# Kernel tuning notes

Measured on AMD Instinct MI355X. Metric: run time of the kernel, lower is better.

## Reference

```python
import jax, jax.numpy as jnp
import numpy as np

B, L, N, C = 8, 33600, 128, 80
ALPHA, BETA, TOPK, EPS = 1.0, 6.0, 13, 1e-9


def setup_inputs() -> dict:
    key = jax.random.key(0)
    ks = jax.random.split(key, 7)
    pred_scores = jax.random.uniform(ks[0], (B, L, C), jnp.float32)  # post-sigmoid scores
    pc = jax.random.uniform(ks[1], (B, L, 2), jnp.float32) * 1024.0
    pwh = jax.random.uniform(ks[2], (B, L, 2), jnp.float32) * 128.0 + 8.0
    pred_boxes = jnp.concatenate([pc - pwh / 2, pc + pwh / 2], axis=-1)  # xyxy
    gc = jax.random.uniform(ks[3], (B, N, 2), jnp.float32) * 1024.0
    gwh = jax.random.uniform(ks[4], (B, N, 2), jnp.float32) * 256.0 + 16.0
    gt_boxes = jnp.concatenate([gc - gwh / 2, gc + gwh / 2], axis=-1)  # xyxy
    anchor_points = jax.random.uniform(ks[5], (1, L, 2), jnp.float32) * 1024.0
    gt_labels = jax.random.randint(ks[6], (B, N, 1), 0, C).astype(jnp.int64)
    # last quarter of GT slots are padding
    pad_gt_mask = (jnp.arange(N)[None, :, None] < 96).astype(jnp.float32)
    pad_gt_mask = jnp.broadcast_to(pad_gt_mask, (B, N, 1))
    return {"pred_scores": pred_scores, "pred_boxes": pred_boxes,
            "anchor_points": anchor_points, "gt_labels": gt_labels,
            "gt_boxes": gt_boxes, "pad_gt_mask": pad_gt_mask, "bg_index": C}


def _pairwise_iou(gt, pr):
    # gt: [B,N,4], pr: [B,L,4] xyxy -> iou [B,N,L]
    lt = jnp.maximum(gt[:, :, None, :2], pr[:, None, :, :2])
    rb = jnp.minimum(gt[:, :, None, 2:], pr[:, None, :, 2:])
    wh = jnp.clip(rb - lt, 0.0)
    inter = wh[..., 0] * wh[..., 1]
    area_g = ((gt[..., 2] - gt[..., 0]) * (gt[..., 3] - gt[..., 1]))[:, :, None]
    area_p = ((pr[..., 2] - pr[..., 0]) * (pr[..., 3] - pr[..., 1]))[:, None, :]
    iou = inter / (area_g + area_p - inter + EPS)
    iou = jnp.where(iou > 1.0 + EPS, 0.0, iou)
    return jnp.clip(jnp.nan_to_num(iou), 0.0, 1.0)


def reference(pred_scores, pred_boxes, anchor_points, gt_labels, gt_boxes, pad_gt_mask, bg_index):
    b, l, c = pred_scores.shape
    n = gt_boxes.shape[1]
    iou = _pairwise_iou(gt_boxes, pred_boxes)  # [B,N,L]

    # spatial containment of anchor points in horizontal gt boxes -> [B,N,L]
    pts = anchor_points[0]  # [L,2]
    spatial = ((pts[None, None, :, 0] >= gt_boxes[:, :, None, 0]) &
               (pts[None, None, :, 0] <= gt_boxes[:, :, None, 2]) &
               (pts[None, None, :, 1] >= gt_boxes[:, :, None, 1]) &
               (pts[None, None, :, 1] <= gt_boxes[:, :, None, 3]))

    # gather per-GT class scores: class_scores[b,n,l] = pred_scores[b,l,label[b,n]]
    lbl = jnp.clip(gt_labels[..., 0], 0, c - 1)  # [B,N]
    ps_t = jnp.transpose(pred_scores, (0, 2, 1))  # [B,C,L]
    class_scores = jnp.take_along_axis(ps_t, jnp.broadcast_to(lbl[:, :, None], (b, n, l)), axis=1)

    align = (class_scores ** ALPHA) * (iou ** BETA)  # [B,N,L]

    # top-k per GT over anchors
    k = min(TOPK, l)
    s = align * spatial.astype(align.dtype)
    _, topk_idx = jax.lax.top_k(s, k)  # [B,N,k]
    bidx = jnp.arange(b)[:, None, None]
    gidx = jnp.arange(n)[None, :, None]
    topk_mask = jnp.zeros((b, n, l), bool).at[bidx, gidx, topk_idx].set(True)
    topk_mask = topk_mask & (pad_gt_mask[..., 0] > 0)[:, :, None]

    positive = topk_mask.astype(align.dtype) * spatial.astype(align.dtype) * pad_gt_mask

    # conflict resolution: anchors matched to >1 GT keep only the best-IoU GT
    conflict = positive.sum(axis=1) > 1  # [B,L]
    best_gt = jnp.argmax(iou, axis=1)  # [B,L]
    best_mask = (jnp.arange(n)[None, :, None] == best_gt[:, None, :])  # [B,N,L]
    positive = jnp.where(conflict[:, None, :], positive * best_mask.astype(positive.dtype), positive)

    has_assign = positive.sum(axis=1) > 0  # [B,L]
    gt_idx = jnp.argmax(positive, axis=1)  # [B,L]
    assigned_labels = jnp.take_along_axis(gt_labels[..., 0], gt_idx, axis=1)  # [B,L]
    assigned_labels = jnp.where(has_assign, assigned_labels, bg_index)
    assigned_boxes = jnp.take_along_axis(gt_boxes, jnp.broadcast_to(gt_idx[:, :, None], (b, l, 4)), axis=1)

    masked_align = align * positive
    max_align = masked_align.max(axis=-1, keepdims=True)  # [B,N,1]
    max_iou = (iou * positive).max(axis=-1, keepdims=True)  # [B,N,1]
    norm_align = masked_align / (max_align + EPS) * max_iou
    norm_factor = norm_align.max(axis=1)  # [B,L]
    # scatter score at assigned class; bg labels (== C) one-hot to all-zero row
    assigned_scores = jax.nn.one_hot(assigned_labels, c, dtype=pred_scores.dtype)
    assigned_scores = assigned_scores * (norm_factor * has_assign.astype(norm_factor.dtype))[:, :, None]
    return assigned_labels, assigned_boxes, assigned_scores
```

## Files before the change

### kernel.cpp

```cpp
#include <hip/hip_runtime.h>
#include <cstdint>
#include <cstddef>

#define B_DIM 8
#define L_DIM 33600
#define N_DIM 128
#define C_DIM 80
#define K_TOP 13
#define EPS_F 1e-9f
#define NCH2 66
#define SEGSZ 32
#define WBUF 352

typedef float f32x4 __attribute__((ext_vector_type(4)));

__device__ __forceinline__ float iou_pair(float g0, float g1, float g2, float g3,
                                          float p0, float p1, float p2, float p3) {
    float ltx = fmaxf(g0, p0), lty = fmaxf(g1, p1);
    float rbx = fminf(g2, p2), rby = fminf(g3, p3);
    float wx = fmaxf(__fsub_rn(rbx, ltx), 0.0f);
    float wy = fmaxf(__fsub_rn(rby, lty), 0.0f);
    float inter = __fmul_rn(wx, wy);
    float ag = __fmul_rn(__fsub_rn(g2, g0), __fsub_rn(g3, g1));
    float ap = __fmul_rn(__fsub_rn(p2, p0), __fsub_rn(p3, p1));
    float den = __fadd_rn(__fsub_rn(__fadd_rn(ag, ap), inter), EPS_F);
    float iou = __fdiv_rn(inter, den);
    if (iou > 1.0f) iou = 0.0f;
    iou = fminf(fmaxf(iou, 0.0f), 1.0f);
    return iou;
}

__device__ __forceinline__ unsigned long long make_key(double s, int l) {
    unsigned long long sb = (unsigned long long)__double_as_longlong(s);
    return (sb & 0xFFFFFFFFFFFF0000ull) | (unsigned long long)(0xFFFF - l);
}

__device__ __forceinline__ void nt_store4(float4 v, float4* p) {
    __builtin_nontemporal_store(*(f32x4*)&v, (f32x4*)p);
}

__global__ __launch_bounds__(256) void k_push(
    const float* __restrict__ pts, const float* __restrict__ pbox,
    const float* __restrict__ gbox, const float* __restrict__ gpad,
    const int* __restrict__ glbl, const float* __restrict__ psc,
    int* __restrict__ scount, unsigned long long* __restrict__ bucket,
    ulonglong2* __restrict__ posb2,
    float* __restrict__ maxal, float* __restrict__ maxio)
{
    const int chunk = blockIdx.x, b = blockIdx.y, t = threadIdx.x;
    __shared__ float4 gb[N_DIM];
    __shared__ int    gli[N_DIM];
    __shared__ int    lcnt[N_DIM];
    if (t < N_DIM) {
        float4 g = reinterpret_cast<const float4*>(gbox)[(size_t)b * N_DIM + t];
        if (gpad[b * N_DIM + t] <= 0.0f) g = make_float4(3e38f, 3e38f, -3e38f, -3e38f);
        gb[t] = g;
        gli[t] = min(max(glbl[b * N_DIM + t], 0), C_DIM - 1);
        lcnt[t] = 0;
        if (chunk == 0) { maxal[b * N_DIM + t] = 0.0f; maxio[b * N_DIM + t] = 0.0f; }
    }
    __syncthreads();

    const float* psb = psc + (size_t)b * L_DIM * C_DIM;
    const float4* pbb = reinterpret_cast<const float4*>(pbox) + (size_t)b * L_DIM;
    const int l0 = chunk * 512 + t, l1 = l0 + 256;
    const bool v0 = (l0 < L_DIM), v1 = (l1 < L_DIM);
    float a0x = -3e38f, a0y = -3e38f, a1x = -3e38f, a1y = -3e38f;
    float4 pb0 = make_float4(0, 0, 0, 0), pb1 = make_float4(0, 0, 0, 0);
    if (v0) {
        posb2[(size_t)b * L_DIM + l0] = make_ulonglong2(0ull, 0ull);
        const float2 ap = reinterpret_cast<const float2*>(pts)[l0];
        a0x = ap.x; a0y = ap.y;
        pb0 = pbb[l0];
    }
    if (v1) {
        posb2[(size_t)b * L_DIM + l1] = make_ulonglong2(0ull, 0ull);
        const float2 ap = reinterpret_cast<const float2*>(pts)[l1];
        a1x = ap.x; a1y = ap.y;
        pb1 = pbb[l1];
    }

    unsigned long long m0a = 0ull, m1a = 0ull, m0b = 0ull, m1b = 0ull;
    for (int n = 0; n < N_DIM; ++n) {
        const float4 g = gb[n];
        bool i0 = (a0x >= g.x && a0x <= g.z && a0y >= g.y && a0y <= g.w);
        bool i1 = (a1x >= g.x && a1x <= g.z && a1y >= g.y && a1y <= g.w);
        if (n < 64) { m0a |= i0 ? (1ull << n) : 0ull;        m0b |= i1 ? (1ull << n) : 0ull; }
        else        { m1a |= i0 ? (1ull << (n - 64)) : 0ull; m1b |= i1 ? (1ull << (n - 64)) : 0ull; }
    }

    const size_t segbase = ((size_t)(b * N_DIM) * NCH2 + chunk) * SEGSZ;
    if (v0 && l0 >= 32) {
        unsigned long long m = m0a;
        while (m) {
            int n = __ffsll((long long)m) - 1; m &= m - 1;
            const float4 g = gb[n];
            float iou = iou_pair(g.x, g.y, g.z, g.w, pb0.x, pb0.y, pb0.z, pb0.w);
            if (iou > 0.0f) {
                float cs = psb[(size_t)l0 * C_DIM + gli[n]];
                double d = (double)iou, d2 = d * d;
                unsigned long long key = make_key((double)cs * (d2 * d2 * d2), l0);
                int pos = atomicAdd(&lcnt[n], 1);
                if (pos < SEGSZ) bucket[segbase + (size_t)n * NCH2 * SEGSZ + pos] = key;
            }
        }
        m = m1a;
        while (m) {
            int n = __ffsll((long long)m) - 1; m &= m - 1;
            const float4 g = gb[n + 64];
            float iou = iou_pair(g.x, g.y, g.z, g.w, pb0.x, pb0.y, pb0.z, pb0.w);
            if (iou > 0.0f) {
                float cs = psb[(size_t)l0 * C_DIM + gli[n + 64]];
                double d = (double)iou, d2 = d * d;
                unsigned long long key = make_key((double)cs * (d2 * d2 * d2), l0);
                int pos = atomicAdd(&lcnt[n + 64], 1);
                if (pos < SEGSZ) bucket[segbase + (size_t)(n + 64) * NCH2 * SEGSZ + pos] = key;
            }
        }
    }
    if (v1) {
        unsigned long long m = m0b;
        while (m) {
            int n = __ffsll((long long)m) - 1; m &= m - 1;
            const float4 g = gb[n];
            float iou = iou_pair(g.x, g.y, g.z, g.w, pb1.x, pb1.y, pb1.z, pb1.w);
            if (iou > 0.0f) {
                float cs = psb[(size_t)l1 * C_DIM + gli[n]];
                double d = (double)iou, d2 = d * d;
                unsigned long long key = make_key((double)cs * (d2 * d2 * d2), l1);
                int pos = atomicAdd(&lcnt[n], 1);
                if (pos < SEGSZ) bucket[segbase + (size_t)n * NCH2 * SEGSZ + pos] = key;
            }
        }
        m = m1b;
        while (m) {
            int n = __ffsll((long long)m) - 1; m &= m - 1;
            const float4 g = gb[n + 64];
            float iou = iou_pair(g.x, g.y, g.z, g.w, pb1.x, pb1.y, pb1.z, pb1.w);
            if (iou > 0.0f) {
                float cs = psb[(size_t)l1 * C_DIM + gli[n + 64]];
                double d = (double)iou, d2 = d * d;
                unsigned long long key = make_key((double)cs * (d2 * d2 * d2), l1);
                int pos = atomicAdd(&lcnt[n + 64], 1);
                if (pos < SEGSZ) bucket[segbase + (size_t)(n + 64) * NCH2 * SEGSZ + pos] = key;
            }
        }
    }
    __syncthreads();

    if (t < N_DIM)
        scount[(b * N_DIM + t) * NCH2 + chunk] = min(lcnt[t], SEGSZ);
}

__global__ __launch_bounds__(256) void k_top13(
    const float* __restrict__ psc, const float* __restrict__ pbox,
    const float* __restrict__ pts, const int* __restrict__ glbl,
    const float* __restrict__ gbox, const float* __restrict__ gpad,
    const int* __restrict__ scount, const unsigned long long* __restrict__ bucket,
    unsigned long long* __restrict__ posbits)
{
    const int t = threadIdx.x, lane = t & 63, wid = t >> 6;
    const int bn = blockIdx.x * 4 + wid;
    const int b = bn >> 7, n = bn & 127;
    const bool active = (gpad[b * N_DIM + n] > 0.0f);

    __shared__ unsigned long long buf[4][WBUF];
    __shared__ int wq[4];
    if (lane == 0) wq[wid] = 0;
    __builtin_amdgcn_wave_barrier();

    if (active) {
        for (int s = lane; s < NCH2; s += 64) {
            int c = scount[bn * NCH2 + s];
            if (c > 0) {
                int pos = atomicAdd(&wq[wid], c);
                const unsigned long long* seg = bucket + ((size_t)bn * NCH2 + s) * SEGSZ;
                for (int j = 0; j < c; ++j)
                    if (pos + j < WBUF) buf[wid][pos + j] = seg[j];
            }
        }
    }
    __syncthreads();
    if (!active) return;

    const int nc = min(wq[wid], WBUF);
    const float g0 = gbox[(b * N_DIM + n) * 4 + 0];
    const float g1 = gbox[(b * N_DIM + n) * 4 + 1];
    const float g2 = gbox[(b * N_DIM + n) * 4 + 2];
    const float g3 = gbox[(b * N_DIM + n) * 4 + 3];
    int lbl = glbl[b * N_DIM + n];
    lbl = min(max(lbl, 0), C_DIM - 1);
    const float* psb = psc + (size_t)b * L_DIM * C_DIM;
    const float* pbb = pbox + (size_t)b * L_DIM * 4;

    unsigned long long key[K_TOP];
    #pragma unroll
    for (int k = 0; k < K_TOP; ++k) key[k] = 0ull;

    if (lane < 32) {
        const int l = lane;
        const float2 ap = reinterpret_cast<const float2*>(pts)[l];
        unsigned long long ck = (unsigned long long)(0xFFFF - l);
        if (ap.x >= g0 && ap.x <= g2 && ap.y >= g1 && ap.y <= g3) {
            const float4 pbv = reinterpret_cast<const float4*>(pbb)[l];
            float iou = iou_pair(g0, g1, g2, g3, pbv.x, pbv.y, pbv.z, pbv.w);
            if (iou > 0.0f) {
                float cs = psb[(size_t)l * C_DIM + lbl];
                double d = (double)iou, d2 = d * d;
                ck = make_key((double)cs * (d2 * d2 * d2), l);
            }
        }
        key[0] = ck;
    }
    for (int i = lane; i < nc; i += 64) {
        unsigned long long ck = buf[wid][i];
        if (ck > key[K_TOP - 1]) {
            #pragma unroll
            for (int k = 0; k < K_TOP; ++k) {
                unsigned long long hi = key[k] > ck ? key[k] : ck;
                unsigned long long lo = key[k] > ck ? ck : key[k];
                key[k] = hi; ck = lo;
            }
        }
    }

    #pragma unroll 1
    for (int r = 0; r < K_TOP; ++r) {
        unsigned long long best = key[0];
        #pragma unroll
        for (int d = 1; d < 64; d <<= 1) {
            unsigned long long o = __shfl_xor(best, d, 64);
            best = o > best ? o : best;
        }
        if (key[0] == best && best != 0ull) {
            #pragma unroll
            for (int k = 0; k < K_TOP - 1; ++k) key[k] = key[k + 1];
            key[K_TOP - 1] = 0ull;
        }
        if (lane == 0) {
            int win = 0xFFFF - (int)(best & 0xFFFFull);
            atomicOr(&posbits[((size_t)b * L_DIM + win) * 2 + (n >> 6)],
                     1ULL << (n & 63));
        }
    }
}

__global__ __launch_bounds__(256) void k_assign(
    const float* __restrict__ psc, const float* __restrict__ pbox,
    const float* __restrict__ pts,
    const int* __restrict__ glbl, const float* __restrict__ gbox,
    const unsigned long long* __restrict__ posbits,
    const int* __restrict__ bgp,
    float* __restrict__ out_lab, float* __restrict__ out_box,
    int* __restrict__ fin_out, float* __restrict__ alat,
    float* __restrict__ maxal, float* __restrict__ maxio)
{
    const int b = blockIdx.y, t = threadIdx.x;
    const int l = blockIdx.x * 256 + t;
    __shared__ float4 gb[N_DIM];
    __shared__ int    gl[N_DIM];
    __shared__ int    qlist[256];
    __shared__ unsigned long long qp0[256], qp1[256];
    __shared__ int    qn;
    if (t == 0) qn = 0;
    if (t < N_DIM) {
        gb[t] = reinterpret_cast<const float4*>(gbox)[(size_t)b * N_DIM + t];
        gl[t] = glbl[b * N_DIM + t];
    }
    __syncthreads();

    if (l < L_DIM) {
        const size_t bl = (size_t)b * L_DIM + l;
        const unsigned long long w0 = posbits[bl * 2 + 0];
        const unsigned long long w1 = posbits[bl * 2 + 1];
        unsigned long long p0 = 0ull, p1 = 0ull;
        if (w0 | w1) {
            const float2 ap = reinterpret_cast<const float2*>(pts)[l];
            unsigned long long m = w0;
            while (m) {
                int n = __ffsll((long long)m) - 1; m &= m - 1;
                float4 g = gb[n];
                if (ap.x >= g.x && ap.x <= g.z && ap.y >= g.y && ap.y <= g.w)
                    p0 |= 1ull << n;
            }
            m = w1;
            while (m) {
                int n = __ffsll((long long)m) - 1; m &= m - 1;
                float4 g = gb[n + 64];
                if (ap.x >= g.x && ap.x <= g.z && ap.y >= g.y && ap.y <= g.w)
                    p1 |= 1ull << n;
            }
        }
        const int pcnt = __popcll(p0) + __popcll(p1);

        if (pcnt <= 1) {
            int fin = (pcnt == 1) ? (p0 ? (__ffsll(p0) - 1) : (64 + __ffsll(p1) - 1)) : -1;
            __builtin_nontemporal_store((fin >= 0) ? (float)gl[fin] : (float)bgp[0], &out_lab[bl]);
            int gidx = (fin >= 0) ? fin : 0;
            nt_store4(gb[gidx], &reinterpret_cast<float4*>(out_box)[bl]);
            fin_out[bl] = fin;
            if (fin >= 0) {
                const float4 pb = reinterpret_cast<const float4*>(pbox)[bl];
                float4 g = gb[fin];
                float iou = iou_pair(g.x, g.y, g.z, g.w, pb.x, pb.y, pb.z, pb.w);
                int lb = min(max(gl[fin], 0), C_DIM - 1);
                float cs = psc[bl * C_DIM + lb];
                float al = cs * powf(iou, 6.0f);
                alat[bl] = al;
                atomicMax((int*)&maxal[b * N_DIM + fin], __float_as_int(al));
                atomicMax((int*)&maxio[b * N_DIM + fin], __float_as_int(iou));
            }
        } else {
            int qi = atomicAdd(&qn, 1);
            qlist[qi] = l; qp0[qi] = p0; qp1[qi] = p1;
        }
    }
    __syncthreads();

    const int lane = t & 63, wid = t >> 6;
    const int nq = qn;
    for (int i = wid; i < nq; i += 4) {
        const int ql = qlist[i];
        const size_t bl = (size_t)b * L_DIM + ql;
        const float4 pb = reinterpret_cast<const float4*>(pbox)[bl];
        float4 gA = gb[lane];
        float4 gB = gb[lane + 64];
        float iouA = iou_pair(gA.x, gA.y, gA.z, gA.w, pb.x, pb.y, pb.z, pb.w);
        float iouB = iou_pair(gB.x, gB.y, gB.z, gB.w, pb.x, pb.y, pb.z, pb.w);
        unsigned long long kA = ((unsigned long long)__float_as_uint(iouA) << 32)
                              | (unsigned long long)(0xFFFFFFFFu - (unsigned)lane);
        unsigned long long kB = ((unsigned long long)__float_as_uint(iouB) << 32)
                              | (unsigned long long)(0xFFFFFFFFu - (unsigned)(lane + 64));
        unsigned long long k = kA > kB ? kA : kB;
        #pragma unroll
        for (int d = 1; d < 64; d <<= 1) {
            unsigned long long o = __shfl_xor(k, d, 64);
            k = o > k ? o : k;
        }
        if (lane == 0) {
            int bestn = (int)(0xFFFFFFFFu - (unsigned)(k & 0xFFFFFFFFull));
            float bestiou = __uint_as_float((unsigned)(k >> 32));
            const unsigned long long p0 = qp0[i], p1 = qp1[i];
            bool posbest = (bestn < 64) ? ((p0 >> bestn) & 1ull) : ((p1 >> (bestn - 64)) & 1ull);
            int fin = posbest ? bestn : -1;
            __builtin_nontemporal_store((fin >= 0) ? (float)gl[fin] : (float)bgp[0], &out_lab[bl]);
            int gidx = (fin >= 0) ? fin : 0;
            nt_store4(gb[gidx], &reinterpret_cast<float4*>(out_box)[bl]);
            fin_out[bl] = fin;
            if (fin >= 0) {
                int lb = min(max(gl[fin], 0), C_DIM - 1);
                float cs = psc[bl * C_DIM + lb];
                float al = cs * powf(bestiou, 6.0f);
                alat[bl] = al;
                atomicMax((int*)&maxal[b * N_DIM + fin], __float_as_int(al));
                atomicMax((int*)&maxio[b * N_DIM + fin], __float_as_int(bestiou));
            }
        }
    }
}

__global__ __launch_bounds__(256) void k_out(
    const int* __restrict__ fin_out, const float* __restrict__ alat,
    const float* __restrict__ maxal, const float* __restrict__ maxio,
    const int* __restrict__ glbl,
    float* __restrict__ outs)
{
    const int APB = 16;
    const int NTILES = (B_DIM * L_DIM + APB - 1) / APB;
    const int t = threadIdx.x;
    __shared__ float snf[APB];
    __shared__ int   scl[APB];
    float4* out4 = reinterpret_cast<float4*>(outs);

    for (int tile = blockIdx.x; tile < NTILES; tile += 2048) {
        const int a0 = tile * APB;
        __syncthreads();
        if (t < APB) {
            int a = a0 + t;
            float v = 0.0f; int c = -1;
            if (a < B_DIM * L_DIM) {
                int b = a / L_DIM;
                int fin = fin_out[a];
                if (fin >= 0) {
                    v = alat[a] / (maxal[b * N_DIM + fin] + EPS_F) * maxio[b * N_DIM + fin];
                    c = glbl[b * N_DIM + fin];
                }
            }
            snf[t] = v; scl[t] = c;
        }
        __syncthreads();
        for (int j = t; j < APB * 20; j += 256) {
            int ai = j / 20;
            int a = a0 + ai;
            if (a >= B_DIM * L_DIM) continue;
            int c0 = (j - ai * 20) * 4;
            float v = snf[ai]; int cl = scl[ai];
            float4 o;
            o.x = (c0 + 0 == cl) ? v : 0.0f;
            o.y = (c0 + 1 == cl) ? v : 0.0f;
            o.z = (c0 + 2 == cl) ? v : 0.0f;
            o.w = (c0 + 3 == cl) ? v : 0.0f;
            nt_store4(o, &out4[(size_t)a * 20 + (j - ai * 20)]);
        }
    }
}

extern "C" void kernel_launch(void* const* d_in, const int* in_sizes, int n_in,
                              void* d_out, int out_size, void* d_ws, size_t ws_size,
                              hipStream_t stream)
{
    const float* psc  = (const float*)d_in[0];
    const float* pbox = (const float*)d_in[1];
    const float* pts  = (const float*)d_in[2];
    const int*   glbl = (const int*)d_in[3];
    const float* gbox = (const float*)d_in[4];
    const float* gpad = (const float*)d_in[5];
    const int*   bgp  = (const int*)d_in[6];

    const size_t P = (size_t)B_DIM * L_DIM * 2 * sizeof(unsigned long long);
    char* w = (char*)d_ws;
    unsigned long long* posbits = (unsigned long long*)w;
    float* maxal = (float*)(w + P);
    float* maxio = (float*)(w + P + 4096);
    int*   scount = (int*) (w + P + 8192);
    int*   fin   = (int*)  (w + P + 8192 + 270336);
    float* alat  = (float*)(w + P + 8192 + 270336 + 1075200);
    unsigned long long* bucket = (unsigned long long*)(w + P + 8192 + 270336 + 2 * 1075200);

    float* out_lab = (float*)d_out;
    float* out_box = out_lab + (size_t)B_DIM * L_DIM;
    float* out_sc  = out_box + (size_t)B_DIM * L_DIM * 4;

    k_push<<<dim3(NCH2, B_DIM), dim3(256), 0, stream>>>(
        pts, pbox, gbox, gpad, glbl, psc, scount, bucket, (ulonglong2*)posbits, maxal, maxio);
    k_top13<<<dim3(256), dim3(256), 0, stream>>>(
        psc, pbox, pts, glbl, gbox, gpad, scount, bucket, posbits);
    k_assign<<<dim3((L_DIM + 255) / 256, B_DIM), dim3(256), 0, stream>>>(
        psc, pbox, pts, glbl, gbox, posbits, bgp,
        out_lab, out_box, fin, alat, maxal, maxio);
    k_out<<<dim3(2048), dim3(256), 0, stream>>>(
        fin, alat, maxal, maxio, glbl, out_sc);
}
```

Before: 75.37 us.

## Zero score output in push kernel and scatter only positives via compact list

```diff
diff --git a/kernel.cpp b/kernel.cpp
--- a/kernel.cpp
+++ b/kernel.cpp
@@ -11,6 +11,7 @@
 #define NCH2 66
 #define SEGSZ 32
 #define WBUF 352
+#define PLCAP 16384
 
 typedef float f32x4 __attribute__((ext_vector_type(4)));
 
@@ -45,7 +46,8 @@
     const int* __restrict__ glbl, const float* __restrict__ psc,
     int* __restrict__ scount, unsigned long long* __restrict__ bucket,
     ulonglong2* __restrict__ posb2,
-    float* __restrict__ maxal, float* __restrict__ maxio)
+    float* __restrict__ maxal, float* __restrict__ maxio,
+    int* __restrict__ pcount, float* __restrict__ out_sc)
 {
     const int chunk = blockIdx.x, b = blockIdx.y, t = threadIdx.x;
     __shared__ float4 gb[N_DIM];
@@ -59,6 +61,7 @@
         lcnt[t] = 0;
         if (chunk == 0) { maxal[b * N_DIM + t] = 0.0f; maxio[b * N_DIM + t] = 0.0f; }
     }
+    if (chunk == 0 && b == 0 && t == 0) *pcount = 0;
     __syncthreads();
 
     const float* psb = psc + (size_t)b * L_DIM * C_DIM;
@@ -150,6 +153,15 @@
 
     if (t < N_DIM)
         scount[(b * N_DIM + t) * NCH2 + chunk] = min(lcnt[t], SEGSZ);
+
+    {
+        const float4 z = make_float4(0.0f, 0.0f, 0.0f, 0.0f);
+        float4* o4 = reinterpret_cast<float4*>(out_sc);
+        const size_t TOT4 = (size_t)B_DIM * L_DIM * (C_DIM / 4);
+        const size_t stride = (size_t)NCH2 * B_DIM * 256;
+        for (size_t i = (size_t)(b * NCH2 + chunk) * 256 + t; i < TOT4; i += stride)
+            nt_store4(z, &o4[i]);
+    }
 }
 
 __global__ __launch_bounds__(256) void k_top13(
@@ -252,8 +264,9 @@
     const unsigned long long* __restrict__ posbits,
     const int* __restrict__ bgp,
     float* __restrict__ out_lab, float* __restrict__ out_box,
-    int* __restrict__ fin_out, float* __restrict__ alat,
-    float* __restrict__ maxal, float* __restrict__ maxio)
+    float* __restrict__ alat,
+    float* __restrict__ maxal, float* __restrict__ maxio,
+    int* __restrict__ pcount, int* __restrict__ plist)
 {
     const int b = blockIdx.y, t = threadIdx.x;
     const int l = blockIdx.x * 256 + t;
@@ -298,7 +311,6 @@
             __builtin_nontemporal_store((fin >= 0) ? (float)gl[fin] : (float)bgp[0], &out_lab[bl]);
             int gidx = (fin >= 0) ? fin : 0;
             nt_store4(gb[gidx], &reinterpret_cast<float4*>(out_box)[bl]);
-            fin_out[bl] = fin;
             if (fin >= 0) {
                 const float4 pb = reinterpret_cast<const float4*>(pbox)[bl];
                 float4 g = gb[fin];
@@ -309,6 +321,8 @@
                 alat[bl] = al;
                 atomicMax((int*)&maxal[b * N_DIM + fin], __float_as_int(al));
                 atomicMax((int*)&maxio[b * N_DIM + fin], __float_as_int(iou));
+                int pi = atomicAdd(pcount, 1);
+                if (pi < PLCAP) plist[pi] = ((int)bl << 7) | fin;
             }
         } else {
             int qi = atomicAdd(&qn, 1);
@@ -346,7 +360,6 @@
             __builtin_nontemporal_store((fin >= 0) ? (float)gl[fin] : (float)bgp[0], &out_lab[bl]);
             int gidx = (fin >= 0) ? fin : 0;
             nt_store4(gb[gidx], &reinterpret_cast<float4*>(out_box)[bl]);
-            fin_out[bl] = fin;
             if (fin >= 0) {
                 int lb = min(max(gl[fin], 0), C_DIM - 1);
                 float cs = psc[bl * C_DIM + lb];
@@ -354,54 +367,30 @@
                 alat[bl] = al;
                 atomicMax((int*)&maxal[b * N_DIM + fin], __float_as_int(al));
                 atomicMax((int*)&maxio[b * N_DIM + fin], __float_as_int(bestiou));
+                int pi = atomicAdd(pcount, 1);
+                if (pi < PLCAP) plist[pi] = ((int)bl << 7) | fin;
             }
         }
     }
 }
 
 __global__ __launch_bounds__(256) void k_out(
-    const int* __restrict__ fin_out, const float* __restrict__ alat,
+    const int* __restrict__ pcount, const int* __restrict__ plist,
+    const float* __restrict__ alat,
     const float* __restrict__ maxal, const float* __restrict__ maxio,
     const int* __restrict__ glbl,
     float* __restrict__ outs)
 {
-    const int APB = 16;
-    const int NTILES = (B_DIM * L_DIM + APB - 1) / APB;
-    const int t = threadIdx.x;
-    __shared__ float snf[APB];
-    __shared__ int   scl[APB];
-    float4* out4 = reinterpret_cast<float4*>(outs);
-
-    for (int tile = blockIdx.x; tile < NTILES; tile += 2048) {
-        const int a0 = tile * APB;
-        __syncthreads();
-        if (t < APB) {
-            int a = a0 + t;
-            float v = 0.0f; int c = -1;
-            if (a < B_DIM * L_DIM) {
-                int b = a / L_DIM;
-                int fin = fin_out[a];
-                if (fin >= 0) {
-                    v = alat[a] / (maxal[b * N_DIM + fin] + EPS_F) * maxio[b * N_DIM + fin];
-                    c = glbl[b * N_DIM + fin];
-                }
-            }
-            snf[t] = v; scl[t] = c;
-        }
-        __syncthreads();
-        for (int j = t; j < APB * 20; j += 256) {
-            int ai = j / 20;
-            int a = a0 + ai;
-            if (a >= B_DIM * L_DIM) continue;
-            int c0 = (j - ai * 20) * 4;
-            float v = snf[ai]; int cl = scl[ai];
-            float4 o;
-            o.x = (c0 + 0 == cl) ? v : 0.0f;
-            o.y = (c0 + 1 == cl) ? v : 0.0f;
-            o.z = (c0 + 2 == cl) ? v : 0.0f;
-            o.w = (c0 + 3 == cl) ? v : 0.0f;
-            nt_store4(o, &out4[(size_t)a * 20 + (j - ai * 20)]);
-        }
+    const int cnt = min(*pcount, PLCAP);
+    for (int i = blockIdx.x * 256 + threadIdx.x; i < cnt; i += 64 * 256) {
+        const int e = plist[i];
+        const int fin = e & 127;
+        const int bl = e >> 7;
+        const int b = bl / L_DIM;
+        float v = alat[bl] / (maxal[b * N_DIM + fin] + EPS_F) * maxio[b * N_DIM + fin];
+        int cl = glbl[b * N_DIM + fin];
+        if (cl >= 0 && cl < C_DIM)
+            outs[(size_t)bl * C_DIM + cl] = v;
     }
 }
 
@@ -423,21 +412,23 @@
     float* maxal = (float*)(w + P);
     float* maxio = (float*)(w + P + 4096);
     int*   scount = (int*) (w + P + 8192);
-    int*   fin   = (int*)  (w + P + 8192 + 270336);
-    float* alat  = (float*)(w + P + 8192 + 270336 + 1075200);
-    unsigned long long* bucket = (unsigned long long*)(w + P + 8192 + 270336 + 2 * 1075200);
+    float* alat  = (float*)(w + P + 8192 + 270336);
+    int*   pcount = (int*) (w + P + 8192 + 270336 + 1075200);
+    int*   plist  = (int*) (w + P + 8192 + 270336 + 1075200 + 4096);
+    unsigned long long* bucket = (unsigned long long*)(w + P + 8192 + 270336 + 1075200 + 4096 + 65536);
 
     float* out_lab = (float*)d_out;
     float* out_box = out_lab + (size_t)B_DIM * L_DIM;
     float* out_sc  = out_box + (size_t)B_DIM * L_DIM * 4;
 
     k_push<<<dim3(NCH2, B_DIM), dim3(256), 0, stream>>>(
-        pts, pbox, gbox, gpad, glbl, psc, scount, bucket, (ulonglong2*)posbits, maxal, maxio);
+        pts, pbox, gbox, gpad, glbl, psc, scount, bucket, (ulonglong2*)posbits,
+        maxal, maxio, pcount, out_sc);
     k_top13<<<dim3(256), dim3(256), 0, stream>>>(
         psc, pbox, pts, glbl, gbox, gpad, scount, bucket, posbits);
     k_assign<<<dim3((L_DIM + 255) / 256, B_DIM), dim3(256), 0, stream>>>(
         psc, pbox, pts, glbl, gbox, posbits, bgp,
-        out_lab, out_box, fin, alat, maxal, maxio);
-    k_out<<<dim3(2048), dim3(256), 0, stream>>>(
-        fin, alat, maxal, maxio, glbl, out_sc);
-}
+        out_lab, out_box, alat, maxal, maxio, pcount, plist);
+    k_out<<<dim3(64), dim3(256), 0, stream>>>(
+        pcount, plist, alat, maxal, maxio, glbl, out_sc);
+}
```

Measured after the change: 103.7 us. +37.6%, slower.
